# Kernel optimization log

Measured on AMD Instinct MI355X. Metric: run time of the kernel, lower is better.

Reference implementation:

```python
import jax, jax.numpy as jnp
import numpy as np

N = 200_000      # nodes
E = 6_400_000    # edges (avg degree 32)
F = 128          # num_node_features
H = 96           # hidden_channels
G = 2_048        # number of graphs in batch


def setup_inputs() -> dict:
    key = jax.random.key(0)
    ks = jax.random.split(key, 12)
    def lin(k, fi, fo):
        kw, kb = jax.random.split(k)
        s = 1.0 / np.sqrt(fi)
        return (jax.random.uniform(kw, (fi, fo), jnp.float32, -s, s),
                jax.random.uniform(kb, (fo,), jnp.float32, -s, s))
    W1, b1 = lin(ks[0], F, H)
    W2, b2 = lin(ks[1], H, H)
    W3, b3 = lin(ks[2], H, H)
    Wl1, bl1 = lin(ks[3], H, H)
    Wl2, bl2 = lin(ks[4], H, 1)
    x = jax.random.normal(ks[5], (N, F), jnp.float32)
    edge_index = jax.random.randint(ks[6], (2, E), 0, N, jnp.int64)
    batch = jnp.sort(jax.random.randint(ks[7], (N,), 0, G, jnp.int64))
    return {"x": x, "W1": W1, "b1": b1, "W2": W2, "b2": b2, "W3": W3, "b3": b3,
            "Wl1": Wl1, "bl1": bl1, "Wl2": Wl2, "bl2": bl2,
            "edge_index": edge_index, "batch": batch}


def _gcn_layer(x, W, b, src, dst, norm):
    # transform then gather-scale-scatter (PyG GCNConv: bias added after aggregation)
    h = x @ W                                     # [N, out]
    msg = h[src] * norm[:, None]                  # [E+N, out]
    out = jax.ops.segment_sum(msg, dst, num_segments=N)
    return out + b


def reference(x, W1, b1, W2, b2, W3, b3, Wl1, bl1, Wl2, bl2, edge_index, batch):
    loops = jnp.arange(N, dtype=edge_index.dtype)
    src = jnp.concatenate([edge_index[0], loops])  # add self loops
    dst = jnp.concatenate([edge_index[1], loops])
    deg = jax.ops.segment_sum(jnp.ones_like(dst, dtype=x.dtype), dst, num_segments=N)
    dinv = jnp.where(deg > 0, deg ** -0.5, 0.0)
    norm = dinv[src] * dinv[dst]                   # symmetric D^-1/2 A D^-1/2

    h = jax.nn.relu(_gcn_layer(x, W1, b1, src, dst, norm))
    h = jax.nn.relu(_gcn_layer(h, W2, b2, src, dst, norm))
    h = _gcn_layer(h, W3, b3, src, dst, norm)
    # dropout(p=0.5) is identity in eval mode

    sums = jax.ops.segment_sum(h, batch, num_segments=G)        # [G, H]
    cnt = jax.ops.segment_sum(jnp.ones((N,), h.dtype), batch, num_segments=G)
    pooled = sums / jnp.maximum(cnt, 1.0)[:, None]              # global_mean_pool

    out = jax.nn.relu(pooled @ Wl1 + bl1)
    out = out @ Wl2 + bl2                                       # [G, 1]
    return out
```

## Files before the change

kernel.cpp:

```cpp
#include <hip/hip_runtime.h>
#include <hip/hip_bf16.h>
#include <hip/hip_fp16.h>
#include <cstdint>
#include <cstddef>
#include <type_traits>


#define H96 96

typedef _Float16 f16x8 __attribute__((ext_vector_type(8)));
typedef float f32x4 __attribute__((ext_vector_type(4)));

static constexpr int NB_SHIFT = 8;
static constexpr int DPB = 1 << NB_SHIFT;
static constexpr int NBMAX = 800;
static constexpr int EPB = 8192;


__global__ __launch_bounds__(256, 4) void k_binscatter(
    const int* __restrict__ src, const int* __restrict__ dst, int E, int nb,
    int cap, int* __restrict__ gfill, unsigned* __restrict__ pairs) {
    __shared__ int cnt[NBMAX];
    const int tid = threadIdx.x;
    for (int b = tid; b < nb; b += 256) cnt[b] = 0;
    __syncthreads();

    const int base = blockIdx.x * EPB;
    int s[32], d[32];
#pragma unroll
    for (int q = 0; q < 32; ++q) {
        const int idx = base + q * 256 + tid;
        if (idx < E) {
            s[q] = src[idx];
            d[q] = dst[idx];
            atomicAdd(&cnt[d[q] >> NB_SHIFT], 1);
        } else {
            d[q] = -1;
        }
    }
    __syncthreads();
    for (int b = tid; b < nb; b += 256) {
        const int c = cnt[b];
        cnt[b] = (c > 0) ? atomicAdd(&gfill[b], c) : 0;
    }
    __syncthreads();
#pragma unroll
    for (int q = 0; q < 32; ++q) {
        if (d[q] >= 0) {
            const int b = d[q] >> NB_SHIFT;
            const int p = atomicAdd(&cnt[b], 1);
            if (p < cap)
                pairs[(size_t)b * cap + p] =
                    (unsigned)(s[q] & 0xFFFFFF) | ((unsigned)(d[q] & (DPB - 1)) << 24);
        }
    }
}

__global__ void k_bstart(const int* __restrict__ gfill, int* __restrict__ bstart, int nb) {
    __shared__ int sm[1024];
    const int tid = threadIdx.x;
    const int v = (tid < nb) ? gfill[tid] : 0;
    sm[tid] = v;
    __syncthreads();
    for (int o = 1; o < 1024; o <<= 1) {
        const int t = (tid >= o) ? sm[tid - o] : 0;
        __syncthreads();
        sm[tid] += t;
        __syncthreads();
    }
    if (tid < nb) bstart[tid] = sm[tid] - v;
    if (tid == 0) bstart[nb] = sm[1023];
}

__global__ __launch_bounds__(256) void k_build2(
    const unsigned* __restrict__ pairs, const int* __restrict__ gfill,
    const int* __restrict__ bstart, int cap, int* __restrict__ rowptr,
    float* __restrict__ dinv, int* __restrict__ csr, int N, int E) {
    __shared__ int cnt2[DPB];
    __shared__ int off2[DPB];
    const int b = blockIdx.x, tid = threadIdx.x;
    const int m = min(gfill[b], cap);
    const unsigned* pb = pairs + (size_t)b * cap;

    cnt2[tid] = 0;
    __syncthreads();
    for (int i = tid; i < m; i += 256) atomicAdd(&cnt2[pb[i] >> 24], 1);
    __syncthreads();

    const int v = cnt2[tid];
    off2[tid] = v;
    __syncthreads();
    for (int o = 1; o < 256; o <<= 1) {
        const int t = (tid >= o) ? off2[tid - o] : 0;
        __syncthreads();
        off2[tid] += t;
        __syncthreads();
    }
    const int excl = off2[tid] - v;
    const int base = bstart[b];
    const int dg = (b << NB_SHIFT) + tid;
    if (dg < N) {
        rowptr[dg] = base + excl;
        dinv[dg] = 1.0f / sqrtf((float)(v + 1));
    }
    if (b == 0 && tid == 0) rowptr[N] = E;
    __syncthreads();
    cnt2[tid] = excl;
    __syncthreads();
    for (int i = tid; i < m; i += 256) {
        const unsigned pk = pb[i];
        const int pos = base + atomicAdd(&cnt2[pk >> 24], 1);
        csr[pos] = (int)(pk & 0xFFFFFF);
    }
}


template <int K, typename AT>
__global__ __launch_bounds__(256) void k_gemm_mfma(const AT* __restrict__ X,
                                                   const float* __restrict__ W,
                                                   const float* __restrict__ dinv,
                                                   __half* __restrict__ Out) {
    __shared__ _Float16 wt[H96][K + 8];
    const int tid = threadIdx.x;
    const int l = tid & 63;
    const int w = tid >> 6;

    for (int idx = tid; idx < K * H96; idx += 256) {
        const int k = idx / H96, j = idx % H96;
        wt[j][k] = (_Float16)W[idx];
    }
    __syncthreads();

    const int g16 = l >> 4;
    const int rl = l & 15;
    const size_t n0 = (size_t)blockIdx.x * 64 + w * 16;

    f32x4 acc[6];
#pragma unroll
    for (int c = 0; c < 6; ++c) acc[c] = (f32x4){0.f, 0.f, 0.f, 0.f};

#pragma unroll
    for (int kk = 0; kk < K / 32; ++kk) {
        const int k0 = kk * 32 + g16 * 8;
        f16x8 a;
        if constexpr (std::is_same<AT, float>::value) {
            const float* xr = X + (n0 + rl) * K + k0;
            const float4 lo = *(const float4*)xr;
            const float4 hi = *(const float4*)(xr + 4);
            a[0] = (_Float16)lo.x; a[1] = (_Float16)lo.y;
            a[2] = (_Float16)lo.z; a[3] = (_Float16)lo.w;
            a[4] = (_Float16)hi.x; a[5] = (_Float16)hi.y;
            a[6] = (_Float16)hi.z; a[7] = (_Float16)hi.w;
        } else {
            a = *(const f16x8*)((const _Float16*)X + (n0 + rl) * K + k0);
        }
#pragma unroll
        for (int c = 0; c < 6; ++c) {
            const f16x8 b = *(const f16x8*)&wt[c * 16 + rl][k0];
            acc[c] = __builtin_amdgcn_mfma_f32_16x16x32_f16(a, b, acc[c], 0, 0, 0);
        }
    }

    const int r0 = g16 * 4;
    float dv[4];
#pragma unroll
    for (int r = 0; r < 4; ++r) dv[r] = dinv[n0 + r0 + r];
#pragma unroll
    for (int c = 0; c < 6; ++c)
#pragma unroll
        for (int r = 0; r < 4; ++r)
            Out[(n0 + r0 + r) * H96 + c * 16 + rl] = __float2half(acc[c][r] * dv[r]);
}


__global__ void k_agg(const __half* __restrict__ g, const int* __restrict__ rowptr,
                      const int* __restrict__ csr, const float* __restrict__ dinv,
                      const float* __restrict__ bias, __half* __restrict__ hout,
                      int N, int RELU) {
    const int d = (blockIdx.x * blockDim.x + threadIdx.x) >> 6;
    if (d >= N) return;
    const int lane = threadIdx.x & 63;
    const int half = lane >> 5;
    const int l = lane & 31;

    float a0, a1, a2;
    if (half == 0) {
        const __half* gr = g + (size_t)d * H96;
        a0 = __half2float(gr[l]);
        a1 = __half2float(gr[l + 32]);
        a2 = __half2float(gr[l + 64]);
    } else {
        a0 = a1 = a2 = 0.0f;
    }
    float b0 = 0.f, b1 = 0.f, b2 = 0.f;
    float c0 = 0.f, c1 = 0.f, c2 = 0.f;
    float e0 = 0.f, e1 = 0.f, e2 = 0.f;

    const int r0 = rowptr[d], r1 = rowptr[d + 1];
    int e = r0 + half;
#pragma unroll 1
    for (; e + 6 < r1; e += 8) {
        const int s0 = csr[e];
        const int s1 = csr[e + 2];
        const int s2 = csr[e + 4];
        const int s3 = csr[e + 6];
        const __half* g0 = g + (size_t)s0 * H96;
        const __half* g1 = g + (size_t)s1 * H96;
        const __half* g2 = g + (size_t)s2 * H96;
        const __half* g3 = g + (size_t)s3 * H96;
        const float v00 = __half2float(g0[l]);
        const float v01 = __half2float(g0[l + 32]);
        const float v02 = __half2float(g0[l + 64]);
        const float v10 = __half2float(g1[l]);
        const float v11 = __half2float(g1[l + 32]);
        const float v12 = __half2float(g1[l + 64]);
        const float v20 = __half2float(g2[l]);
        const float v21 = __half2float(g2[l + 32]);
        const float v22 = __half2float(g2[l + 64]);
        const float v30 = __half2float(g3[l]);
        const float v31 = __half2float(g3[l + 32]);
        const float v32 = __half2float(g3[l + 64]);
        a0 += v00; a1 += v01; a2 += v02;
        b0 += v10; b1 += v11; b2 += v12;
        c0 += v20; c1 += v21; c2 += v22;
        e0 += v30; e1 += v31; e2 += v32;
    }
#pragma unroll 1
    for (; e < r1; e += 2) {
        const int s = csr[e];
        const __half* gs = g + (size_t)s * H96;
        a0 += __half2float(gs[l]);
        a1 += __half2float(gs[l + 32]);
        a2 += __half2float(gs[l + 64]);
    }
    a0 += (b0 + c0) + e0;
    a1 += (b1 + c1) + e1;
    a2 += (b2 + c2) + e2;

    a0 += __shfl_xor(a0, 32);
    a1 += __shfl_xor(a1, 32);
    a2 += __shfl_xor(a2, 32);

    if (half == 0) {
        const float sc = dinv[d];
        float v0 = sc * a0 + bias[l];
        float v1 = sc * a1 + bias[l + 32];
        float v2 = sc * a2 + bias[l + 64];
        if (RELU) { v0 = fmaxf(v0, 0.f); v1 = fmaxf(v1, 0.f); v2 = fmaxf(v2, 0.f); }
        __half* ho = hout + (size_t)d * H96;
        ho[l] = __float2half(v0);
        ho[l + 32] = __float2half(v1);
        ho[l + 64] = __float2half(v2);
    }
}


__global__ void k_pool_head(const __half* __restrict__ h, const int* __restrict__ batch,
                            const float* __restrict__ Wl1, const float* __restrict__ bl1,
                            const float* __restrict__ Wl2, const float* __restrict__ bl2,
                            float* __restrict__ out, int N) {
    const int gph = blockIdx.x;
    const int tid = threadIdx.x;

    int lo = 0, hi = N;
    while (lo < hi) { int mid = (lo + hi) >> 1; if (batch[mid] < gph) lo = mid + 1; else hi = mid; }
    const int seg_lo = lo;
    lo = seg_lo; hi = N;
    while (lo < hi) { int mid = (lo + hi) >> 1; if (batch[mid] < gph + 1) lo = mid + 1; else hi = mid; }
    const int seg_hi = lo;

    __shared__ float pl[H96];
    __shared__ float prod[H96];
    const float inv_cnt = 1.0f / (float)max(seg_hi - seg_lo, 1);
    if (tid < H96) {
        float s = 0.0f;
        for (int n = seg_lo; n < seg_hi; ++n) s += __half2float(h[(size_t)n * H96 + tid]);
        pl[tid] = s * inv_cnt;
    }
    __syncthreads();
    if (tid < H96) {
        float hd = bl1[tid];
        for (int k = 0; k < H96; ++k) hd = fmaf(pl[k], Wl1[k * H96 + tid], hd);
        hd = fmaxf(hd, 0.0f);
        prod[tid] = hd * Wl2[tid];
    }
    __syncthreads();
    if (tid < 32) {
        float v = prod[tid] + prod[tid + 32] + prod[tid + 64];
        for (int o = 16; o; o >>= 1) v += __shfl_down(v, o);
        if (tid == 0) out[gph] = v + bl2[0];
    }
}


extern "C" void kernel_launch(void* const* d_in, const int* in_sizes, int n_in,
                              void* d_out, int out_size, void* d_ws, size_t ws_size,
                              hipStream_t stream) {
    const float* x   = (const float*)d_in[0];
    const float* W1  = (const float*)d_in[1];
    const float* b1  = (const float*)d_in[2];
    const float* W2  = (const float*)d_in[3];
    const float* b2  = (const float*)d_in[4];
    const float* W3  = (const float*)d_in[5];
    const float* b3  = (const float*)d_in[6];
    const float* Wl1 = (const float*)d_in[7];
    const float* bl1 = (const float*)d_in[8];
    const float* Wl2 = (const float*)d_in[9];
    const float* bl2 = (const float*)d_in[10];
    const int*   ei  = (const int*)d_in[11];
    const int*   bat = (const int*)d_in[12];

    const int N = in_sizes[0] / 128;
    const int E = in_sizes[11] / 2;
    const int G = out_size;
    const int* src = ei;
    const int* dst = ei + E;

    const int nb = (N + DPB - 1) >> NB_SHIFT;
    const int avg = E / nb;
    const int cap = (avg + (avg >> 3) + 1024 + 255) & ~255;

    char* wsb = (char*)d_ws;
    size_t off = 0;
    auto alloc = [&](size_t bytes) {
        void* p = wsb + off;
        off += (bytes + 255) & ~(size_t)255;
        return p;
    };
    __half*   g      = (__half*)alloc((size_t)N * H96 * 2);
    __half*   h      = (__half*)alloc((size_t)N * H96 * 2);
    int*      csr    = (int*)alloc((size_t)E * 4);
    int*      rowptr = (int*)alloc((size_t)(N + 1) * 4);
    float*    dinv   = (float*)alloc((size_t)N * 4);
    unsigned* pairs  = (unsigned*)alloc((size_t)nb * cap * 4);
    int*      gfill  = (int*)alloc((size_t)(nb + 1) * 4);
    int*      bstart = (int*)alloc((size_t)(nb + 1) * 4);

    hipMemsetAsync(gfill, 0, (size_t)nb * 4, stream);

    const int bs_blocks = (E + EPB - 1) / EPB;
    k_binscatter<<<bs_blocks, 256, 0, stream>>>(src, dst, E, nb, cap, gfill, pairs);
    k_bstart<<<1, 1024, 0, stream>>>(gfill, bstart, nb);
    k_build2<<<nb, 256, 0, stream>>>(pairs, gfill, bstart, cap, rowptr, dinv, csr, N, E);

    const int gemm_blocks = N / 64;
    const int agg_blocks = (N + 3) / 4;

    k_gemm_mfma<128, float><<<gemm_blocks, 256, 0, stream>>>(x, W1, dinv, g);
    k_agg<<<agg_blocks, 256, 0, stream>>>(g, rowptr, csr, dinv, b1, h, N, 1);
    k_gemm_mfma<96, __half><<<gemm_blocks, 256, 0, stream>>>(h, W2, dinv, g);
    k_agg<<<agg_blocks, 256, 0, stream>>>(g, rowptr, csr, dinv, b2, h, N, 1);
    k_gemm_mfma<96, __half><<<gemm_blocks, 256, 0, stream>>>(h, W3, dinv, g);
    k_agg<<<agg_blocks, 256, 0, stream>>>(g, rowptr, csr, dinv, b3, h, N, 0);

    k_pool_head<<<G, 128, 0, stream>>>(h, bat, Wl1, bl1, Wl2, bl2, (float*)d_out, N);
}
```

Measured before the change: 910.0 us.

## Fuse bin prefix scan into build, halve binscatter tile, parallelize pooling

Drops the separate single-block prefix-scan kernel. Each build block now reduces the preceding bin counts itself to get its base offset, which saves one launch and one serialization point at the cost of redundant reads of gfill. The binscatter tile is halved to 4096 edges per block and the occupancy hint is dropped, giving more blocks and fewer registers per thread. The pooling kernel now splits each graph's node rows across four thread groups, which shortens the serial per-column loop.

```diff
diff --git a/kernel.cpp b/kernel.cpp
--- a/kernel.cpp
+++ b/kernel.cpp
@@ -14,10 +14,10 @@
 static constexpr int NB_SHIFT = 8;
 static constexpr int DPB = 1 << NB_SHIFT;
 static constexpr int NBMAX = 800;
-static constexpr int EPB = 8192;
-
-
-__global__ __launch_bounds__(256, 4) void k_binscatter(
+static constexpr int EPB = 4096;
+
+
+__global__ __launch_bounds__(256) void k_binscatter(
     const int* __restrict__ src, const int* __restrict__ dst, int E, int nb,
     int cap, int* __restrict__ gfill, unsigned* __restrict__ pairs) {
     __shared__ int cnt[NBMAX];
@@ -26,9 +26,9 @@
     __syncthreads();
 
     const int base = blockIdx.x * EPB;
-    int s[32], d[32];
-#pragma unroll
-    for (int q = 0; q < 32; ++q) {
+    int s[16], d[16];
+#pragma unroll
+    for (int q = 0; q < 16; ++q) {
         const int idx = base + q * 256 + tid;
         if (idx < E) {
             s[q] = src[idx];
@@ -45,7 +45,7 @@
     }
     __syncthreads();
 #pragma unroll
-    for (int q = 0; q < 32; ++q) {
+    for (int q = 0; q < 16; ++q) {
         if (d[q] >= 0) {
             const int b = d[q] >> NB_SHIFT;
             const int p = atomicAdd(&cnt[b], 1);
@@ -56,29 +56,25 @@
     }
 }
 
-__global__ void k_bstart(const int* __restrict__ gfill, int* __restrict__ bstart, int nb) {
-    __shared__ int sm[1024];
-    const int tid = threadIdx.x;
-    const int v = (tid < nb) ? gfill[tid] : 0;
-    sm[tid] = v;
-    __syncthreads();
-    for (int o = 1; o < 1024; o <<= 1) {
-        const int t = (tid >= o) ? sm[tid - o] : 0;
-        __syncthreads();
-        sm[tid] += t;
-        __syncthreads();
-    }
-    if (tid < nb) bstart[tid] = sm[tid] - v;
-    if (tid == 0) bstart[nb] = sm[1023];
-}
-
 __global__ __launch_bounds__(256) void k_build2(
     const unsigned* __restrict__ pairs, const int* __restrict__ gfill,
-    const int* __restrict__ bstart, int cap, int* __restrict__ rowptr,
-    float* __restrict__ dinv, int* __restrict__ csr, int N, int E) {
+    int cap, int* __restrict__ rowptr, float* __restrict__ dinv,
+    int* __restrict__ csr, int N, int E, int nb) {
     __shared__ int cnt2[DPB];
     __shared__ int off2[DPB];
+    __shared__ int red[256];
     const int b = blockIdx.x, tid = threadIdx.x;
+
+    int part = 0;
+    for (int i = tid; i < b; i += 256) part += gfill[i];
+    red[tid] = part;
+    __syncthreads();
+    for (int o = 128; o; o >>= 1) {
+        if (tid < o) red[tid] += red[tid + o];
+        __syncthreads();
+    }
+    const int base = red[0];
+
     const int m = min(gfill[b], cap);
     const unsigned* pb = pairs + (size_t)b * cap;
 
@@ -97,7 +93,6 @@
         __syncthreads();
     }
     const int excl = off2[tid] - v;
-    const int base = bstart[b];
     const int dg = (b << NB_SHIFT) + tid;
     if (dg < N) {
         rowptr[dg] = base + excl;
@@ -255,12 +250,15 @@
 }
 
 
-__global__ void k_pool_head(const __half* __restrict__ h, const int* __restrict__ batch,
-                            const float* __restrict__ Wl1, const float* __restrict__ bl1,
-                            const float* __restrict__ Wl2, const float* __restrict__ bl2,
-                            float* __restrict__ out, int N) {
+__global__ __launch_bounds__(384) void k_pool_head(
+    const __half* __restrict__ h, const int* __restrict__ batch,
+    const float* __restrict__ Wl1, const float* __restrict__ bl1,
+    const float* __restrict__ Wl2, const float* __restrict__ bl2,
+    float* __restrict__ out, int N) {
     const int gph = blockIdx.x;
     const int tid = threadIdx.x;
+    const int gr = tid / H96;
+    const int col = tid % H96;
 
     int lo = 0, hi = N;
     while (lo < hi) { int mid = (lo + hi) >> 1; if (batch[mid] < gph) lo = mid + 1; else hi = mid; }
@@ -269,13 +267,19 @@
     while (lo < hi) { int mid = (lo + hi) >> 1; if (batch[mid] < gph + 1) lo = mid + 1; else hi = mid; }
     const int seg_hi = lo;
 
+    __shared__ float part[4][H96];
     __shared__ float pl[H96];
     __shared__ float prod[H96];
+
+    float s = 0.0f;
+    for (int n = seg_lo + gr; n < seg_hi; n += 4)
+        s += __half2float(h[(size_t)n * H96 + col]);
+    part[gr][col] = s;
+    __syncthreads();
+
     const float inv_cnt = 1.0f / (float)max(seg_hi - seg_lo, 1);
     if (tid < H96) {
-        float s = 0.0f;
-        for (int n = seg_lo; n < seg_hi; ++n) s += __half2float(h[(size_t)n * H96 + tid]);
-        pl[tid] = s * inv_cnt;
+        pl[tid] = (part[0][tid] + part[1][tid] + part[2][tid] + part[3][tid]) * inv_cnt;
     }
     __syncthreads();
     if (tid < H96) {
@@ -334,14 +338,12 @@
     float*    dinv   = (float*)alloc((size_t)N * 4);
     unsigned* pairs  = (unsigned*)alloc((size_t)nb * cap * 4);
     int*      gfill  = (int*)alloc((size_t)(nb + 1) * 4);
-    int*      bstart = (int*)alloc((size_t)(nb + 1) * 4);
 
     hipMemsetAsync(gfill, 0, (size_t)nb * 4, stream);
 
     const int bs_blocks = (E + EPB - 1) / EPB;
     k_binscatter<<<bs_blocks, 256, 0, stream>>>(src, dst, E, nb, cap, gfill, pairs);
-    k_bstart<<<1, 1024, 0, stream>>>(gfill, bstart, nb);
-    k_build2<<<nb, 256, 0, stream>>>(pairs, gfill, bstart, cap, rowptr, dinv, csr, N, E);
+    k_build2<<<nb, 256, 0, stream>>>(pairs, gfill, cap, rowptr, dinv, csr, N, E, nb);
 
     const int gemm_blocks = N / 64;
     const int agg_blocks = (N + 3) / 4;
@@ -353,5 +355,5 @@
     k_gemm_mfma<96, __half><<<gemm_blocks, 256, 0, stream>>>(h, W3, dinv, g);
     k_agg<<<agg_blocks, 256, 0, stream>>>(g, rowptr, csr, dinv, b3, h, N, 0);
 
-    k_pool_head<<<G, 128, 0, stream>>>(h, bat, Wl1, bl1, Wl2, bl2, (float*)d_out, N);
-}
+    k_pool_head<<<G, 384, 0, stream>>>(h, bat, Wl1, bl1, Wl2, bl2, (float*)d_out, N);
+}
```

Result: slower. 950.4 us (+4.4%).
